# Optimization experiments

Measured on AMD Instinct MI355X. Metric: run time of the kernel, lower is better.

Reference implementation:

```python
import jax, jax.numpy as jnp
import numpy as np

B, S, MAXP = 4, 512, 64
PATCHES = (16, 32, 64)
P = len(PATCHES)
D, H, L = 384, 6, 4
HD = D // H            # 64 head dim
ROT = HD // 2          # rotary dims: partial_factor (0.0, 0.5)
DFF, E, TOPK = 1536, 8, 2
NSAMP, NVAR = 4, 4
MAXLEN = 512


def rmsnorm(x, w, eps=1e-5):
    return x * jax.lax.rsqrt(jnp.mean(x * x, axis=-1, keepdims=True) + eps) * w


def setup_inputs():
    key = jax.random.key(0)
    ks = iter(jax.random.split(key, 40))

    def nrm(shape, fan_in):
        return jax.random.normal(next(ks), shape, jnp.float32) / np.float32(np.sqrt(fan_in))

    return dict(
        target=jax.random.normal(next(ks), (B, S, MAXP), jnp.float32),
        observed_mask=jnp.ones((B, S, MAXP), bool),
        sample_id=jnp.sort(jax.random.randint(next(ks), (B, S), 0, NSAMP), axis=-1),
        time_id=jnp.sort(jax.random.randint(next(ks), (B, S), 0, MAXLEN), axis=-1),
        variate_id=jax.random.randint(next(ks), (B, S), 0, NVAR),
        prediction_mask=jnp.zeros((B, S), bool),
        patch_idx=jax.random.randint(next(ks), (B, S), 0, P),
        w_in=nrm((P, D, MAXP), MAXP), b_in=jnp.zeros((P, D)),
        w_feat=nrm((P, D, D), D), b_feat=jnp.zeros((P, D)),
        w_res=nrm((P, D, MAXP), MAXP), b_res=jnp.zeros((P, D)),
        norm1_w=jnp.ones((L, D)), norm2_w=jnp.ones((L, D)),
        wq=nrm((L, D, D), D), wk=nrm((L, D, D), D),
        wv=nrm((L, D, D), D), wo=nrm((L, D, D), D),
        qnorm_w=jnp.ones((L, HD)), knorm_w=jnp.ones((L, HD)),
        var_bias=nrm((L, H, 2), 1),
        router_w=nrm((L, E, D), D),
        w1=nrm((L, E, DFF, D), D), w2=nrm((L, E, D, DFF), DFF), w3=nrm((L, E, DFF, D), D),
        final_norm_w=jnp.ones((D,)),
        w_out=nrm((P, 2 * MAXP, D), D), b_out=jnp.zeros((P, 2 * MAXP)),
    )


def _forward(target, observed_mask, sample_id, time_id, variate_id,
             prediction_mask, patch_idx, w_in, b_in, w_feat, b_feat, w_res,
             b_res, norm1_w, norm2_w, wq, wk, wv, wo, qnorm_w, knorm_w,
             var_bias, router_w, w1, w2, w3, final_norm_w, w_out, b_out):
    psz = jnp.array(PATCHES)[patch_idx]                             # [B,S]
    len_mask = jnp.arange(MAXP)[None, None, :] < psz[..., None]     # [B,S,MAXP]

    # ---- PackedStdScaler: mean/std per (batch row, sample_id, variate_id) group ----
    m = (observed_mask & len_mask & ~prediction_mask[..., None]).astype(target.dtype)
    gid = ((jnp.arange(B)[:, None] * NSAMP + sample_id) * NVAR + variate_id).reshape(-1)
    nseg = B * NSAMP * NVAR
    seg = lambda v: jax.ops.segment_sum(v.reshape(-1), gid, num_segments=nseg)
    tobs = jnp.maximum(seg(m.sum(-1)), 1.0)
    loc_g = seg((target * m).sum(-1)) / tobs
    var_g = jnp.maximum(seg((target * target * m).sum(-1)) / tobs - loc_g ** 2, 0.0)
    scale_g = jnp.sqrt(var_g + 1e-5)
    loc = loc_g[gid].reshape(B, S, 1)
    scale = scale_g[gid].reshape(B, S, 1)
    x = (target - loc) / scale * len_mask   # zeroing padded lanes == zero weight cols

    # ---- multi-patch-size projections (per-token weight selection) ----
    oh = jax.nn.one_hot(patch_idx, P, dtype=x.dtype)                # [B,S,P]
    def multi_in(z, w, b):
        y = jnp.einsum('bsi,poi->bspo', z, w) + b[None, None]
        return jnp.einsum('bspo,bsp->bso', y, oh)
    in_r = jax.nn.silu(multi_in(x, w_in, b_in))
    feat = jnp.einsum('bspo,bsp->bso',
                      jnp.einsum('bsd,pod->bspo', in_r, w_feat) + b_feat[None, None], oh)
    h = feat + multi_in(x, w_res, b_res)                            # [B,S,D]

    # ---- packed causal mask, rotary tables, variate bias ----
    attn_mask = (sample_id[:, :, None] == sample_id[:, None, :]) & \
                (time_id[:, :, None] >= time_id[:, None, :])        # [B,Q,K]
    inv_freq = 1.0 / (10000.0 ** (jnp.arange(0, ROT, 2, dtype=jnp.float32) / ROT))
    ang = time_id[..., None].astype(jnp.float32) * inv_freq         # [B,S,ROT/2]
    cos = jnp.cos(ang)[:, :, None, :]
    sin = jnp.sin(ang)[:, :, None, :]

    def rope(z):  # rotary on first ROT head dims, rest pass through
        z1, z2 = z[..., :ROT // 2], z[..., ROT // 2:ROT]
        rot = jnp.concatenate([z1 * cos - z2 * sin, z2 * cos + z1 * sin], -1)
        return jnp.concatenate([rot, z[..., ROT:]], -1)

    var_eq = (variate_id[:, :, None] == variate_id[:, None, :])[:, None]  # [B,1,Q,K]
    T = B * S
    for l in range(L):
        hn = rmsnorm(h, norm1_w[l])
        q = rope(rmsnorm((hn @ wq[l].T).reshape(B, S, H, HD), qnorm_w[l]))
        k = rope(rmsnorm((hn @ wk[l].T).reshape(B, S, H, HD), knorm_w[l]))
        v = (hn @ wv[l].T).reshape(B, S, H, HD)
        scores = jnp.einsum('bqhd,bkhd->bhqk', q, k) / np.float32(np.sqrt(HD))
        bias = jnp.where(var_eq, var_bias[l, :, 0][None, :, None, None],
                         var_bias[l, :, 1][None, :, None, None])
        scores = jnp.where(attn_mask[:, None], scores + bias, -1e9)
        attn = jax.nn.softmax(scores, axis=-1)
        o = jnp.einsum('bhqk,bkhd->bqhd', attn, v).reshape(B, S, D) @ wo[l].T
        h = h + o
        # ---- MoE GLU FFN, top-2 routing ----
        z = rmsnorm(h, norm2_w[l]).reshape(T, D)
        probs = jax.nn.softmax(z @ router_w[l].T, axis=-1)          # [T,E]
        tv, ti = jax.lax.top_k(probs, TOPK)
        tv = tv / tv.sum(-1, keepdims=True)
        gates = jnp.zeros_like(probs).at[jnp.arange(T)[:, None], ti].set(tv)
        a = jax.nn.silu(jnp.einsum('td,efd->tef', z, w1[l])) * \
            jnp.einsum('td,efd->tef', z, w3[l])                      # [T,E,DFF]
        y = jnp.einsum('tef,te,edf->td', a, gates, w2[l])
        h = h + y.reshape(B, S, D)

    h = rmsnorm(h, final_norm_w)
    pp = jnp.einsum('bspo,bsp->bso',
                    jnp.einsum('bsd,pod->bspo', h, w_out) + b_out[None, None], oh)
    mu = pp[..., :MAXP] * scale + loc                               # Normal loc
    sigma = jax.nn.softplus(pp[..., MAXP:]) * scale                 # Normal scale
    return jnp.stack([mu, sigma], axis=0)                           # [2,B,S,MAXP]


def reference(target, observed_mask, sample_id, time_id, variate_id,
              prediction_mask, patch_idx, w_in, b_in, w_feat, b_feat, w_res,
              b_res, norm1_w, norm2_w, wq, wk, wv, wo, qnorm_w, knorm_w,
              var_bias, router_w, w1, w2, w3, final_norm_w, w_out, b_out):
    return _forward(target, observed_mask, sample_id, time_id, variate_id,
                    prediction_mask, patch_idx, w_in, b_in, w_feat, b_feat,
                    w_res, b_res, norm1_w, norm2_w, wq, wk, wv, wo, qnorm_w,
                    knorm_w, var_bias, router_w, w1, w2, w3, final_norm_w,
                    w_out, b_out)
```

## Files before the change

### kernel.cpp

```cpp
#include <hip/hip_runtime.h>
#include <math.h>

constexpr int Bc = 4, Sc = 512, Tn = Bc * Sc;
constexpr int MAXPc = 64;
constexpr int Dc = 384, Hc = 6, HDc = 64, Lc = 4;
constexpr int DFFc = 1536, Ec = 8;
constexpr int NSAMP = 4, NVAR = 4, NSEG = Bc * NSAMP * NVAR;

constexpr size_t F_SEG    = 0;
constexpr size_t F_LOCG   = 192;
constexpr size_t F_SCALEG = 256;
constexpr size_t F_LOCT   = 320;
constexpr size_t F_SCALET = 2368;
constexpr size_t I_CNT    = 4416;
constexpr size_t I_OFF    = 4424;
constexpr size_t I_ASGE   = 4432;
constexpr size_t I_ASGS   = 8528;
constexpr size_t F_ASGG   = 12624;
constexpr size_t I_ROWTOK = 16720;
constexpr size_t F_ROWG   = 20816;
constexpr size_t I_PCNT   = 24912;
constexpr size_t I_POFF   = 24916;
constexpr size_t I_PTOK   = 24920;
constexpr size_t F_H      = 27008;
constexpr size_t F_HN     = F_H   + (size_t)Tn * Dc;
constexpr size_t F_QKV    = F_HN  + (size_t)Tn * Dc;
constexpr size_t F_X      = F_QKV;
constexpr size_t F_INR    = F_QKV + (size_t)Tn * MAXPc;
constexpr size_t F_Q      = F_QKV + (size_t)Tn * 3 * Dc;
constexpr size_t F_K      = F_Q   + (size_t)Tn * Dc;
constexpr size_t F_V      = F_K   + (size_t)Tn * Dc;
constexpr size_t F_O      = F_V   + (size_t)Tn * Dc;
constexpr size_t F_Z      = F_O   + (size_t)Tn * Dc;
constexpr size_t F_ZLO    = F_Z   + (size_t)Tn * Dc / 2;
constexpr size_t F_A      = F_ZLO + (size_t)Tn * Dc / 2;
constexpr size_t F_ALO    = F_A   + (size_t)Tn * DFFc;

typedef __attribute__((ext_vector_type(8))) _Float16 half8v;
typedef __attribute__((ext_vector_type(4))) float f32x4;

#define MFMA16(A, B, C) C = __builtin_amdgcn_mfma_f32_16x16x32_f16(A, B, C, 0, 0, 0)

__device__ __forceinline__ float wred_sum(float v) {
#pragma unroll
  for (int o = 32; o; o >>= 1) v += __shfl_xor(v, o);
  return v;
}

__global__ void k_segstats(const float* __restrict__ target, const int* __restrict__ sample_id,
                           const int* __restrict__ variate_id, const int* __restrict__ patch_idx,
                           float* __restrict__ ws) {
  int row = blockIdx.x * blockDim.x + threadIdx.x;
  if (row >= Tn) return;
  int b = row >> 9;
  int psz = 16 << patch_idx[row];
  const float* t = target + (size_t)row * MAXPc;
  float s1 = 0.f, s2 = 0.f;
  for (int i = 0; i < psz; i++) { float v = t[i]; s1 += v; s2 += v * v; }
  int gid = (b * NSAMP + sample_id[row]) * NVAR + variate_id[row];
  atomicAdd(&ws[F_SEG + gid], (float)psz);
  atomicAdd(&ws[F_SEG + 64 + gid], s1);
  atomicAdd(&ws[F_SEG + 128 + gid], s2);
}

__global__ void k_finalize(float* __restrict__ ws) {
  int g = threadIdx.x;
  if (g < NSEG) {
    float cnt = ws[F_SEG + g], s1 = ws[F_SEG + 64 + g], s2 = ws[F_SEG + 128 + g];
    float tobs = fmaxf(cnt, 1.f);
    float loc = s1 / tobs;
    float var = fmaxf(s2 / tobs - loc * loc, 0.f);
    ws[F_LOCG + g] = loc;
    ws[F_SCALEG + g] = sqrtf(var + 1e-5f);
  }
}

__global__ void k_pgroup(const int* __restrict__ patch_idx, float* __restrict__ ws) {
  __shared__ int cnt[3];
  __shared__ int base[3];
  int tid = threadIdx.x;
  if (tid < 3) cnt[tid] = 0;
  __syncthreads();
  int p0 = patch_idx[tid], p1 = patch_idx[tid + 1024];
  atomicAdd(&cnt[p0], 1);
  atomicAdd(&cnt[p1], 1);
  __syncthreads();
  if (tid == 0) {
    int a = 0;
    int* pc = (int*)ws + I_PCNT;
    int* po = (int*)ws + I_POFF;
// ... 94 lines not shown
      }
    }
  }
}

__global__ __launch_bounds__(256) void k_emb2(float* __restrict__ ws, const float* __restrict__ w_feat,
                                              const float* __restrict__ b_feat) {
  int p = blockIdx.z;
  const int* pc = (const int*)ws + I_PCNT;
  const int* po = (const int*)ws + I_POFF;
  int n_p = pc[p];
  int i0 = blockIdx.y * 64;
  if (i0 >= n_p) return;
  int rowbase = po[p] + i0;
  int n = min(n_p - i0, 64);
  int f0 = blockIdx.x * 64;
  __shared__ float As[64][33];
  __shared__ float Bs[64][33];
  __shared__ int toks[64];
  int tid = threadIdx.x;
  if (tid < 64) toks[tid] = (tid < n) ? ((const int*)ws + I_PTOK)[rowbase + tid] : -1;
  __syncthreads();
  const float* inr = ws + F_INR;
  const float* Bp = w_feat + (size_t)p * Dc * Dc;
  float acc[4][4] = {};
  int ty = tid >> 4, tx = tid & 15;
  for (int k0 = 0; k0 < Dc; k0 += 32) {
#pragma unroll
    for (int u = 0; u < 2; u++) {
      int idx = tid + 256 * u;
      int row = idx >> 3, seg = idx & 7;
      float4 va = (row < n) ? *(const float4*)&inr[(size_t)(rowbase + row) * Dc + k0 + seg * 4]
                            : make_float4(0.f, 0.f, 0.f, 0.f);
      As[row][seg * 4 + 0] = va.x; As[row][seg * 4 + 1] = va.y;
      As[row][seg * 4 + 2] = va.z; As[row][seg * 4 + 3] = va.w;
      float4 vb = *(const float4*)&Bp[(size_t)(f0 + row) * Dc + k0 + seg * 4];
      Bs[row][seg * 4 + 0] = vb.x; Bs[row][seg * 4 + 1] = vb.y;
      Bs[row][seg * 4 + 2] = vb.z; Bs[row][seg * 4 + 3] = vb.w;
    }
    __syncthreads();
#pragma unroll
    for (int kk = 0; kk < 32; kk++) {
      float a[4], b[4];
#pragma unroll
      for (int r = 0; r < 4; r++) a[r] = As[ty * 4 + r][kk];
#pragma unroll
      for (int c = 0; c < 4; c++) b[c] = Bs[tx * 4 + c][kk];
#pragma unroll
      for (int r = 0; r < 4; r++)
#pragma unroll
        for (int c = 0; c < 4; c++) acc[r][c] += a[r] * b[c];
    }
    __syncthreads();
  }
  float* hbuf = ws + F_H;
#pragma unroll
  for (int r = 0; r < 4; r++) {
    int i = ty * 4 + r;
    if (i < n) {
      int tok = toks[i];
#pragma unroll
      for (int c = 0; c < 4; c++) {
        int nn = f0 + tx * 4 + c;
        hbuf[(size_t)tok * Dc + nn] += acc[r][c] + b_feat[p * Dc + nn];
      }
    }
  }
}

__global__ __launch_bounds__(256) void k_rms(const float* __restrict__ src, float* __restrict__ dst,
                                             const float* __restrict__ w) {
  int t = blockIdx.x * 4 + (threadIdx.x >> 6);
  int lane = threadIdx.x & 63;
  float v[6];
  float ss = 0.f;
#pragma unroll
  for (int j = 0; j < 6; j++) { v[j] = src[(size_t)t * Dc + lane + 64 * j]; ss += v[j] * v[j]; }
  ss = wred_sum(ss);
  float rinv = 1.f / sqrtf(ss / Dc + 1e-5f);
#pragma unroll
  for (int j = 0; j < 6; j++) dst[(size_t)t * Dc + lane + 64 * j] = v[j] * rinv * w[lane + 64 * j];
}

__global__ __launch_bounds__(256) void k_qkv_gemm(int l, float* __restrict__ ws,
                                                  const float* __restrict__ wq,
                                                  const float* __restrict__ wk,
                                                  const float* __restrict__ wv) {
  int f0 = blockIdx.x * 64;
  int t0 = blockIdx.y * 64;
  int which = f0 / Dc;
  int r0 = f0 - which * Dc;
  const float* Bp = (which == 0 ? wq : which == 1 ? wk : wv) + (size_t)l * Dc * Dc + (size_t)r0 * Dc;
  const float* Ap = ws + F_HN + (size_t)t0 * Dc;
  __shared__ float As[64][33];
  __shared__ float Bs[64][33];
  float acc[4][4] = {};
  int tid = threadIdx.x, ty = tid >> 4, tx = tid & 15;
  for (int k0 = 0; k0 < Dc; k0 += 32) {
#pragma unroll
    for (int u = 0; u < 2; u++) {
      int idx = tid + 256 * u;
      int row = idx >> 3, seg = idx & 7;
      float4 va = *(const float4*)&Ap[(size_t)row * Dc + k0 + seg * 4];
      As[row][seg * 4 + 0] = va.x; As[row][seg * 4 + 1] = va.y;
      As[row][seg * 4 + 2] = va.z; As[row][seg * 4 + 3] = va.w;
      float4 vb = *(const float4*)&Bp[(size_t)row * Dc + k0 + seg * 4];
      Bs[row][seg * 4 + 0] = vb.x; Bs[row][seg * 4 + 1] = vb.y;
      Bs[row][seg * 4 + 2] = vb.z; Bs[row][seg * 4 + 3] = vb.w;
    }
    __syncthreads();
#pragma unroll
    for (int kk = 0; kk < 32; kk++) {
      float a[4], b[4];
#pragma unroll
      for (int r = 0; r < 4; r++) a[r] = As[ty * 4 + r][kk];
#pragma unroll
      for (int c = 0; c < 4; c++) b[c] = Bs[tx * 4 + c][kk];
#pragma unroll
      for (int r = 0; r < 4; r++)
#pragma unroll
        for (int c = 0; c < 4; c++) acc[r][c] += a[r] * b[c];
    }
    __syncthreads();
  }
  float* qkv = ws + F_QKV;
#pragma unroll
  for (int r = 0; r < 4; r++)
#pragma unroll
    for (int c = 0; c < 4; c++)
      qkv[(size_t)(t0 + ty * 4 + r) * (3 * Dc) + f0 + tx * 4 + c] = acc[r][c];
}

__global__ __launch_bounds__(256) void k_rope(int l, float* __restrict__ ws,
                                              const float* __restrict__ qnw,
                                              const float* __restrict__ knw,
                                              const int* __restrict__ time_id) {
  int w = blockIdx.x * 4 + (threadIdx.x >> 6);
  int lane = threadIdx.x & 63;
  int t = w / Hc, hh = w - (w / Hc) * Hc;
  const float* qkv = ws + F_QKV + (size_t)t * (3 * Dc);
  float qv = qkv[hh * 64 + lane];
  float kv = qkv[Dc + hh * 64 + lane];
  float vv = qkv[2 * Dc + hh * 64 + lane];
  float qs = wred_sum(qv * qv);
  float ks = wred_sum(kv * kv);
  float qn = qv * (1.f / sqrtf(qs / HDc + 1e-5f)) * qnw[l * HDc + lane];
  float kn = kv * (1.f / sqrtf(ks / HDc + 1e-5f)) * knw[l * HDc + lane];
  float qp = __shfl_xor(qn, 16);
  float kp = __shfl_xor(kn, 16);
  float qo = qn, ko = kn;
  if (lane < 32) {
    int j = lane & 15;
    float invf = powf(10000.f, -(float)j / 16.f);
    float ang = (float)time_id[t] * invf;
    float c = cosf(ang), s = sinf(ang);
    if (lane < 16) { qo = qn * c - qp * s; ko = kn * c - kp * s; }
    else           { qo = qn * c + qp * s; ko = kn * c + kp * s; }
  }
  ws[F_Q + (size_t)t * Dc + hh * 64 + lane] = qo;
  ws[F_K + (size_t)t * Dc + hh * 64 + lane] = ko;
  ws[F_V + (size_t)t * Dc + hh * 64 + lane] = vv;
}

__global__ __launch_bounds__(256) void k_flash(int l, float* __restrict__ ws,
                                               const int* __restrict__ sample_id,
                                               const int* __restrict__ time_id,
                                               const int* __restrict__ variate_id,
                                               const float* __restrict__ var_bias) {
  constexpr int PAD = 67;
  __shared__ float Qs[64][PAD];
  __shared__ float Ks[64][PAD];
  __shared__ float Vt[64][PAD];
  __shared__ float Ps[64][PAD];
  __shared__ int sq[64], tq[64], vq[64], sk[64], tk[64], vk[64];
  __shared__ float rowm[64], rowl[64];
  int qt = blockIdx.x, hh = blockIdx.y, b = blockIdx.z;
  int q0 = qt * 64;
  int tbase = b * Sc;
  int tid = threadIdx.x, ty = tid >> 4, tx = tid & 15;
  const float* qb = ws + F_Q;
  const float* kb = ws + F_K;
  const float* vb = ws + F_V;
  for (int idx = tid; idx < 64 * 16; idx += 256) {
    int i = idx >> 4, seg = idx & 15;
    float4 v = *(const float4*)&qb[(size_t)(tbase + q0 + i) * Dc + hh * 64 + seg * 4];
    Qs[i][seg * 4 + 0] = v.x; Qs[i][seg * 4 + 1] = v.y;
    Qs[i][seg * 4 + 2] = v.z; Qs[i][seg * 4 + 3] = v.w;
  }
  if (tid < 64) {
    int t = tbase + q0 + tid;
    sq[tid] = sample_id[t]; tq[tid] = time_id[t]; vq[tid] = variate_id[t];
    rowm[tid] = -1e30f; rowl[tid] = 0.f;
  }
  float b0 = var_bias[(l * Hc + hh) * 2 + 0];
  float b1v = var_bias[(l * Hc + hh) * 2 + 1];
  float Oacc[4][4] = {};
  __syncthreads();
  int smin_q = sq[0], smax_q = sq[63], tmax_q = tq[63];
  for (int kt = 0; kt < 8; kt++) {
    int k0 = kt * 64;
    int smin_k = sample_id[tbase + k0], smax_k = sample_id[tbase + k0 + 63];
    int tmin_k = time_id[tbase + k0];
    if (smin_k > smax_q || smax_k < smin_q || tmin_k > tmax_q) continue;
    __syncthreads();
    for (int idx = tid; idx < 64 * 16; idx += 256) {
      int i = idx >> 4, seg = idx & 15;
      float4 v = *(const float4*)&kb[(size_t)(tbase + k0 + i) * Dc + hh * 64 + seg * 4];
      Ks[i][seg * 4 + 0] = v.x; Ks[i][seg * 4 + 1] = v.y;
      Ks[i][seg * 4 + 2] = v.z; Ks[i][seg * 4 + 3] = v.w;
      float4 w = *(const float4*)&vb[(size_t)(tbase + k0 + i) * Dc + hh * 64 + seg * 4];
      Vt[seg * 4 + 0][i] = w.x; Vt[seg * 4 + 1][i] = w.y;
      Vt[seg * 4 + 2][i] = w.z; Vt[seg * 4 + 3][i] = w.w;
    }
    if (tid < 64) {
      int t = tbase + k0 + tid;
      sk[tid] = sample_id[t]; tk[tid] = time_id[t]; vk[tid] = variate_id[t];
    }
    __syncthreads();
    float s[4][4] = {};
#pragma unroll
    for (int kk = 0; kk < 64; kk++) {
      float a[4], c[4];
#pragma unroll
      for (int r = 0; r < 4; r++) a[r] = Qs[ty * 4 + r][kk];
#pragma unroll
      for (int cc = 0; cc < 4; cc++) c[cc] = Ks[tx * 4 + cc][kk];
#pragma unroll
      for (int r = 0; r < 4; r++)
#pragma unroll
        for (int cc = 0; cc < 4; cc++) s[r][cc] += a[r] * c[cc];
    }
    float fr[4];
#pragma unroll
    for (int r = 0; r < 4; r++) {
      int qi = ty * 4 + r;
      float rmax = -1e30f;
#pragma unroll
      for (int cc = 0; cc < 4; cc++) {
        int ki = tx * 4 + cc;
        bool ok = (sk[ki] == sq[qi]) && (tk[ki] <= tq[qi]);
        float val = ok ? s[r][cc] * 0.125f + ((vk[ki] == vq[qi]) ? b0 : b1v) : -1e9f;
        s[r][cc] = val;
        rmax = fmaxf(rmax, val);
      }
#pragma unroll
      for (int o = 1; o < 16; o <<= 1) rmax = fmaxf(rmax, __shfl_xor(rmax, o));
      float mold = rowm[qi];
      float mnew = fmaxf(mold, rmax);
      float psum = 0.f;
#pragma unroll
      for (int cc = 0; cc < 4; cc++) {
        float pv = __expf(s[r][cc] - mnew);
        s[r][cc] = pv;
        psum += pv;
      }
#pragma unroll
      for (int o = 1; o < 16; o <<= 1) psum += __shfl_xor(psum, o);
      fr[r] = __expf(mold - mnew);
      if (tx == 0) { rowl[qi] = rowl[qi] * fr[r] + psum; rowm[qi] = mnew; }
#pragma unroll
      for (int cc = 0; cc < 4; cc++) Ps[qi][tx * 4 + cc] = s[r][cc];
    }
#pragma unroll
    for (int r = 0; r < 4; r++)
#pragma unroll
      for (int cc = 0; cc < 4; cc++) Oacc[r][cc] *= fr[r];
#pragma unroll
    for (int kk = 0; kk < 64; kk++) {
      float a[4], c[4];
#pragma unroll
      for (int r = 0; r < 4; r++) a[r] = Ps[ty * 4 + r][kk];
#pragma unroll
      for (int cc = 0; cc < 4; cc++) c[cc] = Vt[tx * 4 + cc][kk];
#pragma unroll
      for (int r = 0; r < 4; r++)
#pragma unroll
        for (int cc = 0; cc < 4; cc++) Oacc[r][cc] += a[r] * c[cc];
    }
  }
  float* ob = ws + F_O;
#pragma unroll
  for (int r = 0; r < 4; r++) {
    int qi = ty * 4 + r;
    float inv = 1.f / rowl[qi];
#pragma unroll
    for (int cc = 0; cc < 4; cc++)
      ob[(size_t)(tbase + q0 + qi) * Dc + hh * 64 + tx * 4 + cc] = Oacc[r][cc] * inv;
  }
}

__global__ __launch_bounds__(256) void k_attnout_gemm(int l, float* __restrict__ ws,
                                                      const float* __restrict__ wo) {
  int f0 = blockIdx.x * 64;
  int t0 = blockIdx.y * 64;
  const float* Bp = wo + (size_t)l * Dc * Dc + (size_t)f0 * Dc;
  const float* Ap = ws + F_O + (size_t)t0 * Dc;
  __shared__ float As[64][33];
  __shared__ float Bs[64][33];
  float acc[4][4] = {};
  int tid = threadIdx.x, ty = tid >> 4, tx = tid & 15;
  for (int k0 = 0; k0 < Dc; k0 += 32) {
#pragma unroll
    for (int u = 0; u < 2; u++) {
      int idx = tid + 256 * u;
      int row = idx >> 3, seg = idx & 7;
      float4 va = *(const float4*)&Ap[(size_t)row * Dc + k0 + seg * 4];
      As[row][seg * 4 + 0] = va.x; As[row][seg * 4 + 1] = va.y;
      As[row][seg * 4 + 2] = va.z; As[row][seg * 4 + 3] = va.w;
      float4 vb = *(const float4*)&Bp[(size_t)row * Dc + k0 + seg * 4];
      Bs[row][seg * 4 + 0] = vb.x; Bs[row][seg * 4 + 1] = vb.y;
      Bs[row][seg * 4 + 2] = vb.z; Bs[row][seg * 4 + 3] = vb.w;
    }
    __syncthreads();
#pragma unroll
    for (int kk = 0; kk < 32; kk++) {
      float a[4], b[4];
#pragma unroll
      for (int r = 0; r < 4; r++) a[r] = As[ty * 4 + r][kk];
#pragma unroll
      for (int c = 0; c < 4; c++) b[c] = Bs[tx * 4 + c][kk];
#pragma unroll
      for (int r = 0; r < 4; r++)
#pragma unroll
        for (int c = 0; c < 4; c++) acc[r][c] += a[r] * b[c];
    }
    __syncthreads();
  }
  float* hbuf = ws + F_H;
#pragma unroll
  for (int r = 0; r < 4; r++)
#pragma unroll
    for (int c = 0; c < 4; c++)
      hbuf[(size_t)(t0 + ty * 4 + r) * Dc + f0 + tx * 4 + c] += acc[r][c];
}

__global__ __launch_bounds__(256) void k_router(int l, float* __restrict__ ws,
                                                const float* __restrict__ norm2_w,
                                                const float* __restrict__ router_w) {
  int wid = threadIdx.x >> 6, lane = threadIdx.x & 63;
  int t = blockIdx.x * 4 + wid;
  float* hbuf = ws + F_H;
  _Float16* zh = (_Float16*)(ws + F_Z);
  _Float16* zl = (_Float16*)(ws + F_ZLO);
  float zr[6];
  float ss = 0.f;
#pragma unroll
  for (int j = 0; j < 6; j++) { float v = hbuf[(size_t)t * Dc + lane + 64 * j]; zr[j] = v; ss += v * v; }
  ss = wred_sum(ss);
  float rinv = 1.f / sqrtf(ss / Dc + 1e-5f);
#pragma unroll
  for (int j = 0; j < 6; j++) {
    zr[j] = zr[j] * rinv * norm2_w[l * Dc + lane + 64 * j];
    _Float16 h = (_Float16)zr[j];
    zh[(size_t)t * Dc + lane + 64 * j] = h;
    zl[(size_t)t * Dc + lane + 64 * j] = (_Float16)(zr[j] - (float)h);
  }
  float logits[Ec];
#pragma unroll
  for (int e = 0; e < Ec; e++) {
    const float* rw = router_w + ((size_t)l * Ec + e) * Dc;
    float p = 0.f;
#pragma unroll
    for (int j = 0; j < 6; j++) p += zr[j] * rw[lane + 64 * j];
    logits[e] = wred_sum(p);
  }
  float mx = logits[0];
#pragma unroll
  for (int e = 1; e < Ec; e++) mx = fmaxf(mx, logits[e]);
  float pr[Ec];
#pragma unroll
  for (int e = 0; e < Ec; e++) pr[e] = expf(logits[e] - mx);
  int e0 = 0; float p0 = pr[0];
#pragma unroll
  for (int e = 1; e < Ec; e++) if (pr[e] > p0) { p0 = pr[e]; e0 = e; }
  int e1 = -1; float p1 = -1.f;
#pragma unroll
  for (int e = 0; e < Ec; e++) if (e != e0 && pr[e] > p1) { p1 = pr[e]; e1 = e; }
  float g0 = p0 / (p0 + p1), g1 = p1 / (p0 + p1);
  if (lane == 0) {
    int* cnt = (int*)ws + I_CNT;
    int* ae = (int*)ws + I_ASGE;
    int* as = (int*)ws + I_ASGS;
    float* ag = ws + F_ASGG;
    int s0 = atomicAdd(&cnt[e0], 1); ae[2 * t] = e0; as[2 * t] = s0; ag[2 * t] = g0;
    int s1 = atomicAdd(&cnt[e1], 1); ae[2 * t + 1] = e1; as[2 * t + 1] = s1; ag[2 * t + 1] = g1;
  }
}

__global__ void k_offsets(float* __restrict__ ws) {
  if (threadIdx.x == 0) {
    int* cnt = (int*)ws + I_CNT;
    int* off = (int*)ws + I_OFF;
    int a = 0;
    for (int e = 0; e < Ec; e++) { off[e] = a; a += cnt[e]; }
  }
}

__global__ void k_scatter(float* __restrict__ ws) {
  int idx = blockIdx.x * 256 + threadIdx.x;
  if (idx >= 2 * Tn) return;
  int* ae = (int*)ws + I_ASGE;
  int* as = (int*)ws + I_ASGS;
  float* ag = ws + F_ASGG;
  int* off = (int*)ws + I_OFF;
  int* rt = (int*)ws + I_ROWTOK;
  float* rg = ws + F_ROWG;
  int e = ae[idx];
  int row = off[e] + as[idx];
  rt[row] = idx >> 1;
  rg[row] = ag[idx];
}

constexpr int LPH = 56;

__global__ __launch_bounds__(256) void k_ffn1(int l, float* __restrict__ ws,
                                              const float* __restrict__ w1,
                                              const float* __restrict__ w3) {
  int e = blockIdx.z;
  const int* cnt = (const int*)ws + I_CNT;
  const int* off = (const int*)ws + I_OFF;
  int n_e = cnt[e];
  int i0 = blockIdx.y * 64;
  if (i0 >= n_e) return;
  int rowbase = off[e] + i0;
  int n = min(n_e - i0, 64);
  int f0 = blockIdx.x * 64;
  __shared__ _Float16 Zh[64][LPH], Zl[64][LPH];
  __shared__ _Float16 W1h[64][LPH], W1l[64][LPH];
  __shared__ _Float16 W3h[64][LPH], W3l[64][LPH];
  __shared__ int toks[64];
  int tid = threadIdx.x;
  if (tid < 64) toks[tid] = (tid < n) ? ((const int*)ws + I_ROWTOK)[rowbase + tid] : -1;
  __syncthreads();
  const _Float16* zh = (const _Float16*)(ws + F_Z);
  const _Float16* zl = (const _Float16*)(ws + F_ZLO);
  const float* w1e = w1 + ((size_t)(l * Ec + e)) * DFFc * Dc;
  const float* w3e = w3 + ((size_t)(l * Ec + e)) * DFFc * Dc;
  int wid = tid >> 6, lane = tid & 63;
  int wr = wid >> 1, wc = wid & 1;
  int lrow = lane & 15, lk = (lane >> 4) * 8;
  int srow = tid >> 2, sseg = tid & 3;
  int stok = toks[srow];
  f32x4 acc1[2][2] = {};
  f32x4 acc3[2][2] = {};
  for (int k0 = 0; k0 < Dc; k0 += 32) {
    half8v zv = {}, zlv = {};
    if (stok >= 0) {
      zv  = *(const half8v*)&zh[(size_t)stok * Dc + k0 + sseg * 8];
      zlv = *(const half8v*)&zl[(size_t)stok * Dc + k0 + sseg * 8];
    }
    *(half8v*)&Zh[srow][sseg * 8] = zv;
    *(half8v*)&Zl[srow][sseg * 8] = zlv;
    {
      const float* p = &w1e[(size_t)(f0 + srow) * Dc + k0 + sseg * 8];
      float4 u0 = *(const float4*)p, u1 = *(const float4*)(p + 4);
      float uu[8] = {u0.x, u0.y, u0.z, u0.w, u1.x, u1.y, u1.z, u1.w};
      half8v hh, ll;
#pragma unroll
      for (int j = 0; j < 8; j++) { _Float16 h = (_Float16)uu[j]; hh[j] = h; ll[j] = (_Float16)(uu[j] - (float)h); }
      *(half8v*)&W1h[srow][sseg * 8] = hh;
      *(half8v*)&W1l[srow][sseg * 8] = ll;
    }
    {
      const float* p = &w3e[(size_t)(f0 + srow) * Dc + k0 + sseg * 8];
      float4 u0 = *(const float4*)p, u1 = *(const float4*)(p + 4);
      float uu[8] = {u0.x, u0.y, u0.z, u0.w, u1.x, u1.y, u1.z, u1.w};
      half8v hh, ll;
#pragma unroll
      for (int j = 0; j < 8; j++) { _Float16 h = (_Float16)uu[j]; hh[j] = h; ll[j] = (_Float16)(uu[j] - (float)h); }
      *(half8v*)&W3h[srow][sseg * 8] = hh;
      *(half8v*)&W3l[srow][sseg * 8] = ll;
    }
    __syncthreads();
    half8v ah0 = *(const half8v*)&Zh[wr * 32 + lrow][lk];
    half8v ah1 = *(const half8v*)&Zh[wr * 32 + 16 + lrow][lk];
    half8v al0 = *(const half8v*)&Zl[wr * 32 + lrow][lk];
    half8v al1 = *(const half8v*)&Zl[wr * 32 + 16 + lrow][lk];
    half8v b1h0 = *(const half8v*)&W1h[wc * 32 + lrow][lk];
    half8v b1h1 = *(const half8v*)&W1h[wc * 32 + 16 + lrow][lk];
    half8v b1l0 = *(const half8v*)&W1l[wc * 32 + lrow][lk];
    half8v b1l1 = *(const half8v*)&W1l[wc * 32 + 16 + lrow][lk];
    half8v b3h0 = *(const half8v*)&W3h[wc * 32 + lrow][lk];
    half8v b3h1 = *(const half8v*)&W3h[wc * 32 + 16 + lrow][lk];
    half8v b3l0 = *(const half8v*)&W3l[wc * 32 + lrow][lk];
    half8v b3l1 = *(const half8v*)&W3l[wc * 32 + 16 + lrow][lk];
    MFMA16(ah0, b1h0, acc1[0][0]); MFMA16(ah0, b1l0, acc1[0][0]); MFMA16(al0, b1h0, acc1[0][0]);
    MFMA16(ah0, b1h1, acc1[0][1]); MFMA16(ah0, b1l1, acc1[0][1]); MFMA16(al0, b1h1, acc1[0][1]);
    MFMA16(ah1, b1h0, acc1[1][0]); MFMA16(ah1, b1l0, acc1[1][0]); MFMA16(al1, b1h0, acc1[1][0]);
    MFMA16(ah1, b1h1, acc1[1][1]); MFMA16(ah1, b1l1, acc1[1][1]); MFMA16(al1, b1h1, acc1[1][1]);
    MFMA16(ah0, b3h0, acc3[0][0]); MFMA16(ah0, b3l0, acc3[0][0]); MFMA16(al0, b3h0, acc3[0][0]);
    MFMA16(ah0, b3h1, acc3[0][1]); MFMA16(ah0, b3l1, acc3[0][1]); MFMA16(al0, b3h1, acc3[0][1]);
    MFMA16(ah1, b3h0, acc3[1][0]); MFMA16(ah1, b3l0, acc3[1][0]); MFMA16(al1, b3h0, acc3[1][0]);
    MFMA16(ah1, b3h1, acc3[1][1]); MFMA16(ah1, b3l1, acc3[1][1]); MFMA16(al1, b3h1, acc3[1][1]);
    __syncthreads();
  }
  _Float16* ah = (_Float16*)(ws + F_A);
// ... 137 lines not shown
      As[row][seg * 4 + 2] = va.z; As[row][seg * 4 + 3] = va.w;
      float4 vb = *(const float4*)&Bp[(size_t)row * Dc + k0 + seg * 4];
      Bs[row][seg * 4 + 0] = vb.x; Bs[row][seg * 4 + 1] = vb.y;
      Bs[row][seg * 4 + 2] = vb.z; Bs[row][seg * 4 + 3] = vb.w;
    }
    __syncthreads();
#pragma unroll
    for (int kk = 0; kk < 32; kk++) {
      float a[4], b[4];
#pragma unroll
      for (int r = 0; r < 4; r++) a[r] = As[ty * 4 + r][kk];
#pragma unroll
      for (int c = 0; c < 4; c++) b[c] = Bs[tx * 4 + c][kk];
#pragma unroll
      for (int r = 0; r < 4; r++)
#pragma unroll
        for (int c = 0; c < 4; c++) acc[r][c] += a[r] * b[c];
    }
    __syncthreads();
  }
#pragma unroll
  for (int r = 0; r < 4; r++) {
    int i = ty * 4 + r;
    if (i < n) {
      int tok = toks[i];
      float loc = ws[F_LOCT + tok], scale = ws[F_SCALET + tok];
#pragma unroll
      for (int c = 0; c < 4; c++) {
        int nn = f0 + tx * 4 + c;
        float a = acc[r][c] + b_out[p * 2 * MAXPc + nn];
        if (nn < MAXPc) {
          out[(size_t)tok * MAXPc + nn] = a * scale + loc;
        } else {
          float sp = fmaxf(a, 0.f) + log1pf(expf(-fabsf(a)));
          out[(size_t)Tn * MAXPc + (size_t)tok * MAXPc + (nn - MAXPc)] = sp * scale;
        }
      }
    }
  }
}

extern "C" void kernel_launch(void* const* d_in, const int* in_sizes, int n_in,
                              void* d_out, int out_size, void* d_ws, size_t ws_size,
                              hipStream_t stream) {
  const float* target     = (const float*)d_in[0];
  const int*   sample_id  = (const int*)d_in[2];
  const int*   time_id    = (const int*)d_in[3];
  const int*   variate_id = (const int*)d_in[4];
  const int*   patch_idx  = (const int*)d_in[6];
  const float* w_in   = (const float*)d_in[7];
  const float* b_in   = (const float*)d_in[8];
  const float* w_feat = (const float*)d_in[9];
  const float* b_feat = (const float*)d_in[10];
  const float* w_res  = (const float*)d_in[11];
  const float* b_res  = (const float*)d_in[12];
  const float* norm1_w = (const float*)d_in[13];
  const float* norm2_w = (const float*)d_in[14];
  const float* wq = (const float*)d_in[15];
  const float* wk = (const float*)d_in[16];
  const float* wv = (const float*)d_in[17];
  const float* wo = (const float*)d_in[18];
  const float* qnorm_w = (const float*)d_in[19];
  const float* knorm_w = (const float*)d_in[20];
  const float* var_bias = (const float*)d_in[21];
  const float* router_w = (const float*)d_in[22];
  const float* w1 = (const float*)d_in[23];
  const float* w2 = (const float*)d_in[24];
  const float* w3 = (const float*)d_in[25];
  const float* final_norm_w = (const float*)d_in[26];
  const float* w_out = (const float*)d_in[27];
  const float* b_out = (const float*)d_in[28];

  float* ws = (float*)d_ws;
  float* out = (float*)d_out;

  hipMemsetAsync(ws, 0, 192 * sizeof(float), stream);
  k_segstats<<<8, 256, 0, stream>>>(target, sample_id, variate_id, patch_idx, ws);
  k_finalize<<<1, 64, 0, stream>>>(ws);
  k_pgroup<<<1, 1024, 0, stream>>>(patch_idx, ws);
  k_prep_x<<<Tn / 4, 256, 0, stream>>>(target, sample_id, variate_id, patch_idx, ws);
  k_emb1<<<dim3(6, 32, 3), 256, 0, stream>>>(ws, w_in, b_in, w_res, b_res);
  k_emb2<<<dim3(6, 32, 3), 256, 0, stream>>>(ws, w_feat, b_feat);
  for (int l = 0; l < Lc; l++) {
    k_rms<<<Tn / 4, 256, 0, stream>>>(ws + F_H, ws + F_HN, norm1_w + (size_t)l * Dc);
    k_qkv_gemm<<<dim3(18, 32), 256, 0, stream>>>(l, ws, wq, wk, wv);
    k_rope<<<Tn * Hc / 4, 256, 0, stream>>>(l, ws, qnorm_w, knorm_w, time_id);
    k_flash<<<dim3(8, 6, 4), 256, 0, stream>>>(l, ws, sample_id, time_id, variate_id, var_bias);
    k_attnout_gemm<<<dim3(6, 32), 256, 0, stream>>>(l, ws, wo);
    hipMemsetAsync((int*)ws + I_CNT, 0, Ec * sizeof(int), stream);
    k_router<<<Tn / 4, 256, 0, stream>>>(l, ws, norm2_w, router_w);
    k_offsets<<<1, 64, 0, stream>>>(ws);
    k_scatter<<<(2 * Tn + 255) / 256, 256, 0, stream>>>(ws);
    k_ffn1<<<dim3(DFFc / 64, Tn / 64, Ec), 256, 0, stream>>>(l, ws, w1, w3);
    k_ffn2<<<dim3(12, Tn / 64, Ec), 256, 0, stream>>>(l, ws, w2);
  }
  k_rms<<<Tn / 4, 256, 0, stream>>>(ws + F_H, ws + F_HN, final_norm_w);
  k_head<<<dim3(2, 32, 3), 256, 0, stream>>>(ws, w_out, b_out, out);
}
```

Baseline: 1.818 ms.

## Use split-fp16 MFMA for QKV/out projections and split-K flash attention

QKV and attention-output GEMMs now use fp16 MFMA with hi/lo split operands (three MFMAs per tile), replacing scalar fp32 FMA loops. The RMS norm writes split fp16 activations directly. Flash attention is split over KSPLIT key chunks to raise the block count from 192 to 768, and a new combine kernel merges the partial softmax states and emits split-fp16 output for the projection. This adds an extra kernel launch and partial-buffer traffic, and split-fp16 precision is slightly below fp32; skipped key tiles leave rowm at -1e30 for the combine step.

After: 1.677 ms. -7.8%, faster.

```diff
diff --git a/kernel.cpp b/kernel.cpp
--- a/kernel.cpp
+++ b/kernel.cpp
@@ -6,6 +6,7 @@
 constexpr int Dc = 384, Hc = 6, HDc = 64, Lc = 4;
 constexpr int DFFc = 1536, Ec = 8;
 constexpr int NSAMP = 4, NVAR = 4, NSEG = Bc * NSAMP * NVAR;
+constexpr int KSPLIT = 4;
 
 constexpr size_t F_SEG    = 0;
 constexpr size_t F_LOCG   = 192;
@@ -266,7 +267,30 @@
   for (int j = 0; j < 6; j++) dst[(size_t)t * Dc + lane + 64 * j] = v[j] * rinv * w[lane + 64 * j];
 }
 
-__global__ __launch_bounds__(256) void k_qkv_gemm(int l, float* __restrict__ ws,
+__global__ __launch_bounds__(256) void k_rms_split(float* __restrict__ ws, const float* __restrict__ w) {
+  int t = blockIdx.x * 4 + (threadIdx.x >> 6);
+  int lane = threadIdx.x & 63;
+  const float* src = ws + F_H;
+  _Float16* Hh = (_Float16*)(ws + F_HN);
+  _Float16* Hl = Hh + (size_t)Tn * Dc;
+  float v[6];
+  float ss = 0.f;
+#pragma unroll
+  for (int j = 0; j < 6; j++) { v[j] = src[(size_t)t * Dc + lane + 64 * j]; ss += v[j] * v[j]; }
+  ss = wred_sum(ss);
+  float rinv = 1.f / sqrtf(ss / Dc + 1e-5f);
+#pragma unroll
+  for (int j = 0; j < 6; j++) {
+    float y = v[j] * rinv * w[lane + 64 * j];
+    _Float16 h = (_Float16)y;
+    Hh[(size_t)t * Dc + lane + 64 * j] = h;
+    Hl[(size_t)t * Dc + lane + 64 * j] = (_Float16)(y - (float)h);
+  }
+}
+
+constexpr int LPH = 56;
+
+__global__ __launch_bounds__(256) void k_qkv_cf16(int l, float* __restrict__ ws,
                                                   const float* __restrict__ wq,
                                                   const float* __restrict__ wk,
                                                   const float* __restrict__ wv) {
@@ -275,44 +299,54 @@
   int which = f0 / Dc;
   int r0 = f0 - which * Dc;
   const float* Bp = (which == 0 ? wq : which == 1 ? wk : wv) + (size_t)l * Dc * Dc + (size_t)r0 * Dc;
-  const float* Ap = ws + F_HN + (size_t)t0 * Dc;
-  __shared__ float As[64][33];
-  __shared__ float Bs[64][33];
-  float acc[4][4] = {};
-  int tid = threadIdx.x, ty = tid >> 4, tx = tid & 15;
+  const _Float16* Hh = (const _Float16*)(ws + F_HN);
+  const _Float16* Hl = Hh + (size_t)Tn * Dc;
+  __shared__ _Float16 Ahs[64][LPH], Als[64][LPH];
+  __shared__ _Float16 Bhs[64][LPH], Bls[64][LPH];
+  int tid = threadIdx.x, wid = tid >> 6, lane = tid & 63;
+  int wr = wid >> 1, wc = wid & 1;
+  int lrow = lane & 15, lk = (lane >> 4) * 8;
+  int srow = tid >> 2, sseg = tid & 3;
+  f32x4 acc[2][2] = {};
   for (int k0 = 0; k0 < Dc; k0 += 32) {
-#pragma unroll
-    for (int u = 0; u < 2; u++) {
-      int idx = tid + 256 * u;
-      int row = idx >> 3, seg = idx & 7;
-      float4 va = *(const float4*)&Ap[(size_t)row * Dc + k0 + seg * 4];
-      As[row][seg * 4 + 0] = va.x; As[row][seg * 4 + 1] = va.y;
-      As[row][seg * 4 + 2] = va.z; As[row][seg * 4 + 3] = va.w;
-      float4 vb = *(const float4*)&Bp[(size_t)row * Dc + k0 + seg * 4];
-      Bs[row][seg * 4 + 0] = vb.x; Bs[row][seg * 4 + 1] = vb.y;
-      Bs[row][seg * 4 + 2] = vb.z; Bs[row][seg * 4 + 3] = vb.w;
-    }
-    __syncthreads();
-#pragma unroll
-    for (int kk = 0; kk < 32; kk++) {
-      float a[4], b[4];
-#pragma unroll
-      for (int r = 0; r < 4; r++) a[r] = As[ty * 4 + r][kk];
-#pragma unroll
-      for (int c = 0; c < 4; c++) b[c] = Bs[tx * 4 + c][kk];
-#pragma unroll
-      for (int r = 0; r < 4; r++)
-#pragma unroll
-        for (int c = 0; c < 4; c++) acc[r][c] += a[r] * b[c];
-    }
+    *(half8v*)&Ahs[srow][sseg * 8] = *(const half8v*)&Hh[(size_t)(t0 + srow) * Dc + k0 + sseg * 8];
+    *(half8v*)&Als[srow][sseg * 8] = *(const half8v*)&Hl[(size_t)(t0 + srow) * Dc + k0 + sseg * 8];
+    const float* p = &Bp[(size_t)srow * Dc + k0 + sseg * 8];
+    float4 u0 = *(const float4*)p, u1 = *(const float4*)(p + 4);
+    float uu[8] = {u0.x, u0.y, u0.z, u0.w, u1.x, u1.y, u1.z, u1.w};
+    half8v hh, ll;
+#pragma unroll
+    for (int j = 0; j < 8; j++) { _Float16 h = (_Float16)uu[j]; hh[j] = h; ll[j] = (_Float16)(uu[j] - (float)h); }
+    *(half8v*)&Bhs[srow][sseg * 8] = hh;
+    *(half8v*)&Bls[srow][sseg * 8] = ll;
+    __syncthreads();
+    half8v a0h = *(const half8v*)&Ahs[wr * 32 + lrow][lk];
+    half8v a1h = *(const half8v*)&Ahs[wr * 32 + 16 + lrow][lk];
+    half8v a0l = *(const half8v*)&Als[wr * 32 + lrow][lk];
+    half8v a1l = *(const half8v*)&Als[wr * 32 + 16 + lrow][lk];
+    half8v b0h = *(const half8v*)&Bhs[wc * 32 + lrow][lk];
+    half8v b1h = *(const half8v*)&Bhs[wc * 32 + 16 + lrow][lk];
+    half8v b0l = *(const half8v*)&Bls[wc * 32 + lrow][lk];
+    half8v b1l = *(const half8v*)&Bls[wc * 32 + 16 + lrow][lk];
+    MFMA16(a0h, b0h, acc[0][0]); MFMA16(a0h, b0l, acc[0][0]); MFMA16(a0l, b0h, acc[0][0]);
+    MFMA16(a0h, b1h, acc[0][1]); MFMA16(a0h, b1l, acc[0][1]); MFMA16(a0l, b1h, acc[0][1]);
+    MFMA16(a1h, b0h, acc[1][0]); MFMA16(a1h, b0l, acc[1][0]); MFMA16(a1l, b0h, acc[1][0]);
+    MFMA16(a1h, b1h, acc[1][1]); MFMA16(a1h, b1l, acc[1][1]); MFMA16(a1l, b1h, acc[1][1]);
     __syncthreads();
   }
   float* qkv = ws + F_QKV;
 #pragma unroll
-  for (int r = 0; r < 4; r++)
-#pragma unroll
-    for (int c = 0; c < 4; c++)
-      qkv[(size_t)(t0 + ty * 4 + r) * (3 * Dc) + f0 + tx * 4 + c] = acc[r][c];
+  for (int fi = 0; fi < 2; fi++) {
+#pragma unroll
+    for (int ii = 0; ii < 4; ii++) {
+      int rtile = wr * 32 + fi * 16 + (lane >> 4) * 4 + ii;
+#pragma unroll
+      for (int fj = 0; fj < 2; fj++) {
+        int col = f0 + wc * 32 + fj * 16 + lrow;
+        qkv[(size_t)(t0 + rtile) * (3 * Dc) + col] = acc[fi][fj][ii];
+      }
+    }
+  }
 }
 
 __global__ __launch_bounds__(256) void k_rope(int l, float* __restrict__ ws,
@@ -358,7 +392,9 @@
   __shared__ float Ps[64][PAD];
   __shared__ int sq[64], tq[64], vq[64], sk[64], tk[64], vk[64];
   __shared__ float rowm[64], rowl[64];
-  int qt = blockIdx.x, hh = blockIdx.y, b = blockIdx.z;
+  int qt = blockIdx.x, ksid = blockIdx.y;
+  int hb = blockIdx.z;
+  int b = hb / Hc, hh = hb - b * Hc;
   int q0 = qt * 64;
   int tbase = b * Sc;
   int tid = threadIdx.x, ty = tid >> 4, tx = tid & 15;
@@ -381,7 +417,9 @@
   float Oacc[4][4] = {};
   __syncthreads();
   int smin_q = sq[0], smax_q = sq[63], tmax_q = tq[63];
-  for (int kt = 0; kt < 8; kt++) {
+  constexpr int KT_PER = 8 / KSPLIT;
+  for (int j = 0; j < KT_PER; j++) {
+    int kt = ksid * KT_PER + j;
     int k0 = kt * 64;
     int smin_k = sample_id[tbase + k0], smax_k = sample_id[tbase + k0 + 63];
     int tmin_k = time_id[tbase + k0];
@@ -462,60 +500,102 @@
         for (int cc = 0; cc < 4; cc++) Oacc[r][cc] += a[r] * c[cc];
     }
   }
-  float* ob = ws + F_O;
+  float* PO = ws + F_A;
+  float* PM = ws + F_ALO;
+  float* PL = PM + (size_t)KSPLIT * Tn * Hc;
 #pragma unroll
   for (int r = 0; r < 4; r++) {
     int qi = ty * 4 + r;
-    float inv = 1.f / rowl[qi];
 #pragma unroll
     for (int cc = 0; cc < 4; cc++)
-      ob[(size_t)(tbase + q0 + qi) * Dc + hh * 64 + tx * 4 + cc] = Oacc[r][cc] * inv;
-  }
-}
-
-__global__ __launch_bounds__(256) void k_attnout_gemm(int l, float* __restrict__ ws,
+      PO[((size_t)ksid * Tn + tbase + q0 + qi) * Dc + hh * 64 + tx * 4 + cc] = Oacc[r][cc];
+  }
+  __syncthreads();
+  if (tid < 64) {
+    size_t o = ((size_t)ksid * Tn + tbase + q0 + tid) * Hc + hh;
+    PM[o] = rowm[tid];
+    PL[o] = rowl[tid];
+  }
+}
+
+__global__ __launch_bounds__(256) void k_fcomb(float* __restrict__ ws) {
+  int w = blockIdx.x * 4 + (threadIdx.x >> 6);
+  int lane = threadIdx.x & 63;
+  int t = w / Hc, hh = w - (w / Hc) * Hc;
+  const float* PO = ws + F_A;
+  const float* PM = ws + F_ALO;
+  const float* PL = PM + (size_t)KSPLIT * Tn * Hc;
+  float m = -1e30f;
+#pragma unroll
+  for (int k = 0; k < KSPLIT; k++) m = fmaxf(m, PM[((size_t)k * Tn + t) * Hc + hh]);
+  float lsum = 0.f, o = 0.f;
+#pragma unroll
+  for (int k = 0; k < KSPLIT; k++) {
+    float wgt = __expf(PM[((size_t)k * Tn + t) * Hc + hh] - m);
+    lsum += PL[((size_t)k * Tn + t) * Hc + hh] * wgt;
+    o += PO[((size_t)k * Tn + t) * Dc + hh * 64 + lane] * wgt;
+  }
+  float r = o / lsum;
+  _Float16* Oh = (_Float16*)(ws + F_O);
+  _Float16* Ol = Oh + (size_t)Tn * Dc;
+  _Float16 hv = (_Float16)r;
+  Oh[(size_t)t * Dc + hh * 64 + lane] = hv;
+  Ol[(size_t)t * Dc + hh * 64 + lane] = (_Float16)(r - (float)hv);
+}
+
+__global__ __launch_bounds__(256) void k_attnout_cf16(int l, float* __restrict__ ws,
                                                       const float* __restrict__ wo) {
   int f0 = blockIdx.x * 64;
   int t0 = blockIdx.y * 64;
   const float* Bp = wo + (size_t)l * Dc * Dc + (size_t)f0 * Dc;
-  const float* Ap = ws + F_O + (size_t)t0 * Dc;
-  __shared__ float As[64][33];
-  __shared__ float Bs[64][33];
-  float acc[4][4] = {};
-  int tid = threadIdx.x, ty = tid >> 4, tx = tid & 15;
+  const _Float16* Oh = (const _Float16*)(ws + F_O);
+  const _Float16* Ol = Oh + (size_t)Tn * Dc;
+  __shared__ _Float16 Ahs[64][LPH], Als[64][LPH];
+  __shared__ _Float16 Bhs[64][LPH], Bls[64][LPH];
+  int tid = threadIdx.x, wid = tid >> 6, lane = tid & 63;
+  int wr = wid >> 1, wc = wid & 1;
+  int lrow = lane & 15, lk = (lane >> 4) * 8;
+  int srow = tid >> 2, sseg = tid & 3;
+  f32x4 acc[2][2] = {};
   for (int k0 = 0; k0 < Dc; k0 += 32) {
-#pragma unroll
-    for (int u = 0; u < 2; u++) {
-      int idx = tid + 256 * u;
-      int row = idx >> 3, seg = idx & 7;
-      float4 va = *(const float4*)&Ap[(size_t)row * Dc + k0 + seg * 4];
-      As[row][seg * 4 + 0] = va.x; As[row][seg * 4 + 1] = va.y;
-      As[row][seg * 4 + 2] = va.z; As[row][seg * 4 + 3] = va.w;
-      float4 vb = *(const float4*)&Bp[(size_t)row * Dc + k0 + seg * 4];
-      Bs[row][seg * 4 + 0] = vb.x; Bs[row][seg * 4 + 1] = vb.y;
-      Bs[row][seg * 4 + 2] = vb.z; Bs[row][seg * 4 + 3] = vb.w;
-    }
-    __syncthreads();
-#pragma unroll
-    for (int kk = 0; kk < 32; kk++) {
-      float a[4], b[4];
-#pragma unroll
-      for (int r = 0; r < 4; r++) a[r] = As[ty * 4 + r][kk];
-#pragma unroll
-      for (int c = 0; c < 4; c++) b[c] = Bs[tx * 4 + c][kk];
-#pragma unroll
-      for (int r = 0; r < 4; r++)
-#pragma unroll
-        for (int c = 0; c < 4; c++) acc[r][c] += a[r] * b[c];
-    }
+    *(half8v*)&Ahs[srow][sseg * 8] = *(const half8v*)&Oh[(size_t)(t0 + srow) * Dc + k0 + sseg * 8];
+    *(half8v*)&Als[srow][sseg * 8] = *(const half8v*)&Ol[(size_t)(t0 + srow) * Dc + k0 + sseg * 8];
+    const float* p = &Bp[(size_t)srow * Dc + k0 + sseg * 8];
+    float4 u0 = *(const float4*)p, u1 = *(const float4*)(p + 4);
+    float uu[8] = {u0.x, u0.y, u0.z, u0.w, u1.x, u1.y, u1.z, u1.w};
+    half8v hh, ll;
+#pragma unroll
+    for (int j = 0; j < 8; j++) { _Float16 h = (_Float16)uu[j]; hh[j] = h; ll[j] = (_Float16)(uu[j] - (float)h); }
+    *(half8v*)&Bhs[srow][sseg * 8] = hh;
+    *(half8v*)&Bls[srow][sseg * 8] = ll;
+    __syncthreads();
+    half8v a0h = *(const half8v*)&Ahs[wr * 32 + lrow][lk];
+    half8v a1h = *(const half8v*)&Ahs[wr * 32 + 16 + lrow][lk];
+    half8v a0l = *(const half8v*)&Als[wr * 32 + lrow][lk];
+    half8v a1l = *(const half8v*)&Als[wr * 32 + 16 + lrow][lk];
+    half8v b0h = *(const half8v*)&Bhs[wc * 32 + lrow][lk];
+    half8v b1h = *(const half8v*)&Bhs[wc * 32 + 16 + lrow][lk];
+    half8v b0l = *(const half8v*)&Bls[wc * 32 + lrow][lk];
+    half8v b1l = *(const half8v*)&Bls[wc * 32 + 16 + lrow][lk];
+    MFMA16(a0h, b0h, acc[0][0]); MFMA16(a0h, b0l, acc[0][0]); MFMA16(a0l, b0h, acc[0][0]);
+    MFMA16(a0h, b1h, acc[0][1]); MFMA16(a0h, b1l, acc[0][1]); MFMA16(a0l, b1h, acc[0][1]);
+    MFMA16(a1h, b0h, acc[1][0]); MFMA16(a1h, b0l, acc[1][0]); MFMA16(a1l, b0h, acc[1][0]);
+    MFMA16(a1h, b1h, acc[1][1]); MFMA16(a1h, b1l, acc[1][1]); MFMA16(a1l, b1h, acc[1][1]);
     __syncthreads();
   }
   float* hbuf = ws + F_H;
 #pragma unroll
-  for (int r = 0; r < 4; r++)
-#pragma unroll
-    for (int c = 0; c < 4; c++)
-      hbuf[(size_t)(t0 + ty * 4 + r) * Dc + f0 + tx * 4 + c] += acc[r][c];
+  for (int fi = 0; fi < 2; fi++) {
+#pragma unroll
+    for (int ii = 0; ii < 4; ii++) {
+      int rtile = wr * 32 + fi * 16 + (lane >> 4) * 4 + ii;
+#pragma unroll
+      for (int fj = 0; fj < 2; fj++) {
+        int col = f0 + wc * 32 + fj * 16 + lrow;
+        hbuf[(size_t)(t0 + rtile) * Dc + col] += acc[fi][fj][ii];
+      }
+    }
+  }
 }
 
 __global__ __launch_bounds__(256) void k_router(int l, float* __restrict__ ws,
@@ -594,8 +674,6 @@
   rt[row] = idx >> 1;
   rg[row] = ag[idx];
 }
-
-constexpr int LPH = 56;
 
 __global__ __launch_bounds__(256) void k_ffn1(int l, float* __restrict__ ws,
                                               const float* __restrict__ w1,
@@ -899,11 +977,12 @@
   k_emb1<<<dim3(6, 32, 3), 256, 0, stream>>>(ws, w_in, b_in, w_res, b_res);
   k_emb2<<<dim3(6, 32, 3), 256, 0, stream>>>(ws, w_feat, b_feat);
   for (int l = 0; l < Lc; l++) {
-    k_rms<<<Tn / 4, 256, 0, stream>>>(ws + F_H, ws + F_HN, norm1_w + (size_t)l * Dc);
-    k_qkv_gemm<<<dim3(18, 32), 256, 0, stream>>>(l, ws, wq, wk, wv);
+    k_rms_split<<<Tn / 4, 256, 0, stream>>>(ws, norm1_w + (size_t)l * Dc);
+    k_qkv_cf16<<<dim3(18, 32), 256, 0, stream>>>(l, ws, wq, wk, wv);
     k_rope<<<Tn * Hc / 4, 256, 0, stream>>>(l, ws, qnorm_w, knorm_w, time_id);
-    k_flash<<<dim3(8, 6, 4), 256, 0, stream>>>(l, ws, sample_id, time_id, variate_id, var_bias);
-    k_attnout_gemm<<<dim3(6, 32), 256, 0, stream>>>(l, ws, wo);
+    k_flash<<<dim3(8, KSPLIT, 24), 256, 0, stream>>>(l, ws, sample_id, time_id, variate_id, var_bias);
+    k_fcomb<<<Tn * Hc / 4, 256, 0, stream>>>(ws);
+    k_attnout_cf16<<<dim3(6, 32), 256, 0, stream>>>(l, ws, wo);
     hipMemsetAsync((int*)ws + I_CNT, 0, Ec * sizeof(int), stream);
     k_router<<<Tn / 4, 256, 0, stream>>>(l, ws, norm2_w, router_w);
     k_offsets<<<1, 64, 0, stream>>>(ws);
```
